# Kernel optimization log

Measured on AMD Instinct MI355X. Metric: run time of the kernel, lower is better.

The kernel has to match this reference:

```python
import jax, jax.numpy as jnp
import numpy as np

V = 100000
E = 1600000
BN_EPS = 1e-5


def spmm(edge_index, vals, X):
    # X: (V, Cin, B); sparse L @ X via scatter-add. y[r] += w * X[c]
    rows, cols = edge_index[0], edge_index[1]
    return jnp.zeros_like(X).at[rows].add(vals[:, None, None] * X[cols])


def cheb_conv(x, edge_index, vals, w, b=None):
    # x: (B, Cin, V), w: (K, Cin, Cout) -> (B, Cout, V)
    K = w.shape[0]
    x0 = jnp.transpose(x, (2, 1, 0))  # (V, Cin, B)
    xs = [x0]
    if K > 1:
        x1 = spmm(edge_index, vals, x0)
        xs.append(x1)
        for _ in range(2, K):
            x2 = 2.0 * spmm(edge_index, vals, x1) - x0
            xs.append(x2)
            x0, x1 = x1, x2
    xk = jnp.stack(xs)  # (K, V, Cin, B)
    out = jnp.einsum('kvcb,kco->bov', xk, w)
    if b is not None:
        out = out + b[None, :, None]
    return out


def batch_norm(x, g, b):
    # training-mode BatchNorm1d on (B, C, V): stats over (B, V), biased var
    m = jnp.mean(x, axis=(0, 2), keepdims=True)
    v = jnp.var(x, axis=(0, 2), keepdims=True)
    return g[None, :, None] * (x - m) * jax.lax.rsqrt(v + BN_EPS) + b[None, :, None]


def setup_inputs() -> dict:
    key = jax.random.key(0)
    ks = jax.random.split(key, 8)
    x = jax.random.normal(ks[0], (4, 32, V), dtype=jnp.float32)
    edge_index = jax.random.randint(ks[1], (2, E), 0, V, dtype=jnp.int32)
    # small values keep the K=4 Chebyshev recursion well-scaled
    lap_vals = 0.1 * jax.random.normal(ks[2], (E,), dtype=jnp.float32)
    def w(k, K, cin, cout):
        s = 1.0 / np.sqrt(K * cin)
        return s * jax.random.normal(k, (K, cin, cout), dtype=jnp.float32)
    return {
        'x': x, 'edge_index': edge_index, 'lap_vals': lap_vals,
        'in_bn_g': jnp.ones((32,), jnp.float32), 'in_bn_b': jnp.zeros((32,), jnp.float32),
        'in_w': w(ks[3], 4, 32, 64), 'in_b': jnp.zeros((64,), jnp.float32),
        'h0_bn_g': jnp.ones((64,), jnp.float32), 'h0_bn_b': jnp.zeros((64,), jnp.float32),
        'h0_w': w(ks[4], 4, 64, 64), 'h0_b': jnp.zeros((64,), jnp.float32),
        'h1_bn_g': jnp.ones((64,), jnp.float32), 'h1_bn_b': jnp.zeros((64,), jnp.float32),
        'h1_w': w(ks[5], 4, 64, 32), 'h1_b': jnp.zeros((32,), jnp.float32),
    }


def reference(x, edge_index, lap_vals, in_bn_g, in_bn_b, in_w, in_b,
              h0_bn_g, h0_bn_b, h0_w, h0_b, h1_bn_g, h1_bn_b, h1_w, h1_b):
    xn = batch_norm(x, in_bn_g, in_bn_b)
    out = cheb_conv(xn, edge_index, lap_vals, in_w, in_b)
    # hidden layer 0
    out = jax.nn.relu(out)
    out = batch_norm(out, h0_bn_g, h0_bn_b)
    out = cheb_conv(out, edge_index, lap_vals, h0_w, h0_b)
    # hidden layer 1
    out = jax.nn.relu(out)
    out = batch_norm(out, h1_bn_g, h1_bn_b)
    out = cheb_conv(out, edge_index, lap_vals, h1_w, h1_b)
    # in_channels == out_channels -> Identity shortcut on the BN'ed input
    return jax.nn.relu(out + xn)
```

## Files before the change

kernel.cpp:

```cpp
#include <hip/hip_runtime.h>
#include <cstdint>
#include <cstddef>

#define VN 100000
#define EN 1600000
static constexpr float BN_EPS_F = 1e-5f;
static constexpr float INV_N = 1.0f / 400000.0f;

using short8 = __attribute__((ext_vector_type(8))) short;
using f32x4  = __attribute__((ext_vector_type(4))) float;

__device__ __forceinline__ float bf_lo(unsigned int p) {
  return __builtin_bit_cast(float, p << 16);
}
__device__ __forceinline__ float bf_hi(unsigned int p) {
  return __builtin_bit_cast(float, p & 0xffff0000u);
}
__device__ __forceinline__ float bf1(unsigned short u) {
  return __builtin_bit_cast(float, ((unsigned int)u) << 16);
}
__device__ __forceinline__ unsigned short f2bf(float f) {
  unsigned int x = __builtin_bit_cast(unsigned int, f);
  x += 0x7fffu + ((x >> 16) & 1u);
  return (unsigned short)(x >> 16);
}
__device__ __forceinline__ unsigned int pack2(float a, float b) {
  return (unsigned int)f2bf(a) | ((unsigned int)f2bf(b) << 16);
}

template <int EPL, bool AX>
__device__ __forceinline__ void gather_accum(int start, int end,
    const int* __restrict__ cs, const float* __restrict__ vs,
    const unsigned short* __restrict__ X, int XS, int lane,
    float4 sc, float4 sh, float* acc) {
  int e = start;
  if constexpr (EPL == 4) {
    for (; e + 8 <= end; e += 8) {
      uint2 q[8]; float w[8];
#pragma unroll
      for (int u = 0; u < 8; u++) {
        q[u] = *reinterpret_cast<const uint2*>(X + (size_t)cs[e + u] * XS + lane * 4);
        w[u] = vs[e + u];
      }
#pragma unroll
      for (int u = 0; u < 8; u++) {
        float v0 = bf_lo(q[u].x), v1 = bf_hi(q[u].x), v2 = bf_lo(q[u].y), v3 = bf_hi(q[u].y);
        if constexpr (AX) {
          v0 = fmaxf(v0, 0.f) * sc.x + sh.x;
          v1 = fmaxf(v1, 0.f) * sc.y + sh.y;
          v2 = fmaxf(v2, 0.f) * sc.z + sh.z;
          v3 = fmaxf(v3, 0.f) * sc.w + sh.w;
        }
        acc[0] += w[u] * v0; acc[1] += w[u] * v1;
        acc[2] += w[u] * v2; acc[3] += w[u] * v3;
      }
    }
    for (; e + 4 <= end; e += 4) {
      uint2 q[4]; float w[4];
#pragma unroll
      for (int u = 0; u < 4; u++) {
        q[u] = *reinterpret_cast<const uint2*>(X + (size_t)cs[e + u] * XS + lane * 4);
        w[u] = vs[e + u];
      }
#pragma unroll
      for (int u = 0; u < 4; u++) {
        float v0 = bf_lo(q[u].x), v1 = bf_hi(q[u].x), v2 = bf_lo(q[u].y), v3 = bf_hi(q[u].y);
        if constexpr (AX) {
          v0 = fmaxf(v0, 0.f) * sc.x + sh.x;
          v1 = fmaxf(v1, 0.f) * sc.y + sh.y;
          v2 = fmaxf(v2, 0.f) * sc.z + sh.z;
          v3 = fmaxf(v3, 0.f) * sc.w + sh.w;
        }
        acc[0] += w[u] * v0; acc[1] += w[u] * v1;
        acc[2] += w[u] * v2; acc[3] += w[u] * v3;
      }
    }
    for (; e < end; e++) {
      const uint2 q = *reinterpret_cast<const uint2*>(X + (size_t)cs[e] * XS + lane * 4);
      const float w = vs[e];
      float v0 = bf_lo(q.x), v1 = bf_hi(q.x), v2 = bf_lo(q.y), v3 = bf_hi(q.y);
      if constexpr (AX) {
        v0 = fmaxf(v0, 0.f) * sc.x + sh.x;
        v1 = fmaxf(v1, 0.f) * sc.y + sh.y;
        v2 = fmaxf(v2, 0.f) * sc.z + sh.z;
        v3 = fmaxf(v3, 0.f) * sc.w + sh.w;
      }
      acc[0] += w * v0; acc[1] += w * v1; acc[2] += w * v2; acc[3] += w * v3;
    }
  } else {
    for (; e + 8 <= end; e += 8) {
      unsigned int q[8]; float w[8];
#pragma unroll
      for (int u = 0; u < 8; u++) {
        q[u] = *reinterpret_cast<const unsigned int*>(X + (size_t)cs[e + u] * XS + lane * 2);
        w[u] = vs[e + u];
      }
#pragma unroll
      for (int u = 0; u < 8; u++) {
        acc[0] += w[u] * bf_lo(q[u]);
        acc[1] += w[u] * bf_hi(q[u]);
      }
    }
    for (; e + 4 <= end; e += 4) {
      unsigned int q[4]; float w[4];
#pragma unroll
      for (int u = 0; u < 4; u++) {
        q[u] = *reinterpret_cast<const unsigned int*>(X + (size_t)cs[e + u] * XS + lane * 2);
        w[u] = vs[e + u];
      }
#pragma unroll
      for (int u = 0; u < 4; u++) {
        acc[0] += w[u] * bf_lo(q[u]);
        acc[1] += w[u] * bf_hi(q[u]);
      }
    }
    for (; e < end; e++) {
      const unsigned int q = *reinterpret_cast<const unsigned int*>(X + (size_t)cs[e] * XS + lane * 2);
      const float w = vs[e];
      acc[0] += w * bf_lo(q);
      acc[1] += w * bf_hi(q);
    }
  }
}

__global__ __launch_bounds__(256) void stats_x_kernel(const float* __restrict__ x,
                                                      float* __restrict__ stats) {
  const int p = blockIdx.x & 127;
  const int chunk = blockIdx.x >> 7;
  const int c = p & 31, b = p >> 5;
  const float* base = x + ((size_t)b * 32 + c) * VN + chunk * 12500;
  float s = 0.f, s2 = 0.f;
  for (int i = threadIdx.x; i < 12500; i += 256) {
    float v = base[i];
    s += v; s2 += v * v;
  }
  __shared__ float r1[256], r2[256];
  r1[threadIdx.x] = s; r2[threadIdx.x] = s2;
  __syncthreads();
  for (int off = 128; off > 0; off >>= 1) {
    if (threadIdx.x < off) {
      r1[threadIdx.x] += r1[threadIdx.x + off];
      r2[threadIdx.x] += r2[threadIdx.x + off];
    }
    __syncthreads();
  }
  if (threadIdx.x == 0) {
    atomicAdd(&stats[c], r1[0]);
    atomicAdd(&stats[64 + c], r2[0]);
  }
}

__global__ void finalize_stats_kernel(float* __restrict__ stats,
                                      const float* __restrict__ g,
                                      const float* __restrict__ beta, int C) {
  int c = threadIdx.x;
  if (c < C) {
    float m = stats[c] * INV_N;
    float var = stats[64 + c] * INV_N - m * m;
    float sc = g[c] * rsqrtf(var + BN_EPS_F);
    stats[128 + c] = sc;
    stats[192 + c] = beta[c] - m * sc;
  }
}

__global__ __launch_bounds__(128) void bn_transpose_kernel(const float* __restrict__ x,
                                                           const float* __restrict__ stats,
                                                           unsigned short* __restrict__ xn) {
  const int tid = threadIdx.x;
  const int b = tid >> 5, c = tid & 31;
  const int v0 = blockIdx.x * 64;
  const float sc = stats[128 + c], sh = stats[192 + c];
  const float* src = x + ((size_t)b * 32 + c) * VN;
  for (int i = 0; i < 64; i++) {
    int v = v0 + i;
    if (v < VN) xn[(size_t)v * 128 + tid] = f2bf(sc * src[v] + sh);
  }
}

__global__ __launch_bounds__(256) void pack_wb_kernel(const float* __restrict__ W,
                                                      unsigned short* __restrict__ Wb,
                                                      int Cin, int Cout) {
  const int i = blockIdx.x * 256 + threadIdx.x;
  const int KC = Cin >> 5, T = Cout >> 4;
  const int tot = 4 * KC * T * 512;
  if (i >= tot) return;
  const int j = i & 7;
  const int l = (i >> 3) & 63;
  const int rem = i >> 9;
  const int t = rem % T;
  const int kc = (rem / T) % KC;
  const int k = rem / (T * KC);
  const int c = kc * 32 + (l >> 4) * 8 + j;
  const int o = t * 16 + (l & 15);
  Wb[i] = f2bf(W[((size_t)k * Cin + c) * Cout + o]);
}

__global__ __launch_bounds__(256) void hist_kernel(const int* __restrict__ rows,
                                                   int* __restrict__ cnt) {
  int i = blockIdx.x * blockDim.x + threadIdx.x;
  const int stride = gridDim.x * blockDim.x;
  for (; i < EN; i += stride) atomicAdd(&cnt[rows[i]], 1);
}

__global__ __launch_bounds__(256) void scan1_kernel(const int* __restrict__ cnt,
                                                    int* __restrict__ rp,
                                                    int* __restrict__ chunkSums) {
  __shared__ int sh[256];
  const int t = threadIdx.x;
  const int base = blockIdx.x * 2048 + t * 8;
  int vals[8]; int tot = 0;
#pragma unroll
  for (int i = 0; i < 8; i++) {
    int idx = base + i;
    int v = (idx < VN) ? cnt[idx] : 0;
    vals[i] = v; tot += v;
  }
  sh[t] = tot;
  __syncthreads();
  for (int off = 1; off < 256; off <<= 1) {
    int v = (t >= off) ? sh[t - off] : 0;
    __syncthreads();
    sh[t] += v;
    __syncthreads();
  }
  int run = sh[t] - tot;
#pragma unroll
  for (int i = 0; i < 8; i++) {
    int idx = base + i;
    if (idx < VN) rp[idx] = run;
    run += vals[i];
  }
  if (t == 255) chunkSums[blockIdx.x] = sh[255];
}

__global__ void scan2_kernel(const int* __restrict__ chunkSums,
                             int* __restrict__ chunkOff,
                             int* __restrict__ rp, int nChunks) {
  if (threadIdx.x == 0 && blockIdx.x == 0) {
    int off = 0;
    for (int j = 0; j < nChunks; j++) { chunkOff[j] = off; off += chunkSums[j]; }
    rp[VN] = off;
  }
}

__global__ __launch_bounds__(256) void scan3_kernel(int* __restrict__ rp,
                                                    const int* __restrict__ chunkOff,
                                                    int* __restrict__ fill) {
  int i = blockIdx.x * 256 + threadIdx.x;
  if (i < VN) {
    int v = rp[i] + chunkOff[i >> 11];
    rp[i] = v;
    fill[i] = v;
  }
}

__global__ __launch_bounds__(256) void fill_kernel(const int* __restrict__ rows,
                                                   const int* __restrict__ cols,
                                                   const float* __restrict__ lap,
                                                   int* __restrict__ fill,
                                                   int* __restrict__ cols_s,
                                                   float* __restrict__ vals_s) {
  int i = blockIdx.x * blockDim.x + threadIdx.x;
  const int stride = gridDim.x * blockDim.x;
  for (; i < EN; i += stride) {
    int r = rows[i];
    int pos = atomicAdd(&fill[r], 1);
    cols_s[pos] = cols[i];
    vals_s[pos] = lap[i];
  }
}

template <int EPL, int MODE, bool AX, bool AP>
__global__ __launch_bounds__(256, 8) void spmm_kernel(const int* __restrict__ rp,
                                                   const int* __restrict__ cs,
                                                   const float* __restrict__ vs,
                                                   const unsigned short* __restrict__ X, int XS,
                                                   const unsigned short* __restrict__ P, int PS,
                                                   const unsigned short* __restrict__ Q, int QS,
                                                   unsigned short* __restrict__ Y, int YS,
                                                   const float* __restrict__ bnp) {
  const int lane = threadIdx.x & 63;
  const int row = blockIdx.x * 4 + (threadIdx.x >> 6);
  const int start = rp[row], end = rp[row + 1];
  float4 sc = {0.f, 0.f, 0.f, 0.f}, sh = {0.f, 0.f, 0.f, 0.f};
  if constexpr (AX || AP) {
    const int c0 = (lane * 4) & 63;
    sc = *reinterpret_cast<const float4*>(bnp + c0);
    sh = *reinterpret_cast<const float4*>(bnp + 64 + c0);
  }
  float acc[EPL];
#pragma unroll
  for (int j = 0; j < EPL; j++) acc[j] = 0.f;
  gather_accum<EPL, AX>(start, end, cs, vs, X, XS, lane, sc, sh, acc);

  if constexpr (EPL == 4) {
    float r0 = acc[0], r1 = acc[1], r2 = acc[2], r3 = acc[3];
    if constexpr (MODE == 1) {
      const uint2 p = *reinterpret_cast<const uint2*>(P + (size_t)row * PS + lane * 4);
      float p0 = bf_lo(p.x), p1 = bf_hi(p.x), p2 = bf_lo(p.y), p3 = bf_hi(p.y);
      if constexpr (AP) {
        p0 = fmaxf(p0, 0.f) * sc.x + sh.x;
        p1 = fmaxf(p1, 0.f) * sc.y + sh.y;
        p2 = fmaxf(p2, 0.f) * sc.z + sh.z;
        p3 = fmaxf(p3, 0.f) * sc.w + sh.w;
      }
      r0 = 2.f * r0 - p0;
      r1 = 2.f * r1 - p1;
      r2 = 2.f * r2 - p2;
      r3 = 2.f * r3 - p3;
    }
    uint2 r;
    r.x = pack2(r0, r1);
    r.y = pack2(r2, r3);
    *reinterpret_cast<uint2*>(Y + (size_t)row * YS + lane * 4) = r;
  } else {
    float r0 = acc[0], r1 = acc[1];
    if constexpr (MODE == 1) {
      const unsigned int p = *reinterpret_cast<const unsigned int*>(P + (size_t)row * PS + lane * 2);
      r0 = 2.f * r0 - bf_lo(p);
      r1 = 2.f * r1 - bf_hi(p);
    } else if constexpr (MODE == 2) {
      const unsigned int p = *reinterpret_cast<const unsigned int*>(P + (size_t)row * PS + lane * 2);
      r0 = 2.f * r0 + bf_lo(p);
      r1 = 2.f * r1 + bf_hi(p);
    } else if constexpr (MODE == 3) {
      const unsigned int p = *reinterpret_cast<const unsigned int*>(P + (size_t)row * PS + lane * 2);
      const unsigned int qq = *reinterpret_cast<const unsigned int*>(Q + (size_t)row * QS + lane * 2);
      r0 = 2.f * r0 - bf_lo(qq) + bf_lo(p);
      r1 = 2.f * r1 - bf_hi(qq) + bf_hi(p);
    } else if constexpr (MODE == 4) {
      const unsigned int p = *reinterpret_cast<const unsigned int*>(P + (size_t)row * PS + lane * 2);
      const unsigned int qq = *reinterpret_cast<const unsigned int*>(Q + (size_t)row * QS + lane * 2);
      r0 = r0 - bf_lo(qq) + bf_lo(p);
      r1 = r1 - bf_hi(qq) + bf_hi(p);
    }
    *reinterpret_cast<unsigned int*>(Y + (size_t)row * YS + lane * 2) = pack2(r0, r1);
  }
}

template <int Cin, int Cout, int X0S, int X1S, int X2S, bool AFF0>
__global__ __launch_bounds__(256, 8) void fused_cheb_kernel(const int* __restrict__ rp,
                                                         const int* __restrict__ cs,
                                                         const float* __restrict__ vs,
                                                         const unsigned short* __restrict__ X0,
                                                         const unsigned short* __restrict__ X1,
                                                         const unsigned short* __restrict__ X2,
                                                         unsigned short* __restrict__ OUT,
                                                         const unsigned short* __restrict__ Wb,
                                                         const float* __restrict__ Bias,
                                                         const float* __restrict__ bnp) {
  constexpr int EPL = Cin * 4 / 64;
  constexpr int ROWSH = Cin * 4;
  __shared__ unsigned short t3s[4 * ROWSH];
  const int lane = threadIdx.x & 63;
  const int wv = threadIdx.x >> 6;
  const int row0 = blockIdx.x * 4;
  const int row = row0 + wv;

  float g[EPL];
#pragma unroll
  for (int j = 0; j < EPL; j++) g[j] = 0.f;
  const int start = rp[row], end = rp[row + 1];
  const float4 z4 = {0.f, 0.f, 0.f, 0.f};
  gather_accum<EPL, false>(start, end, cs, vs, X2, X2S, lane, z4, z4, g);
  {
    unsigned int* tw = reinterpret_cast<unsigned int*>(t3s + wv * ROWSH);
    if constexpr (EPL == 4) {
      const uint2 p = *reinterpret_cast<const uint2*>(X1 + (size_t)row * X1S + lane * 4);
      tw[lane * 2]     = pack2(2.f * g[0] - bf_lo(p.x), 2.f * g[1] - bf_hi(p.x));
      tw[lane * 2 + 1] = pack2(2.f * g[2] - bf_lo(p.y), 2.f * g[3] - bf_hi(p.y));
    } else {
      const unsigned int p = *reinterpret_cast<const unsigned int*>(X1 + (size_t)row * X1S + lane * 2);
      tw[lane] = pack2(2.f * g[0] - bf_lo(p), 2.f * g[1] - bf_hi(p));
    }
  }
  __syncthreads();

  constexpr int KC = Cin / 32;
  constexpr int T = Cout / 16;
  const int col = lane & 15, quad = lane >> 4;
  const int t = wv % T;
  const int ar = col >> 2, ab = col & 3;

  const unsigned short* xa0 = X0 + (size_t)(row0 + ar) * X0S + ab * Cin + quad * 8;
  const unsigned short* xa1 = X1 + (size_t)(row0 + ar) * X1S + ab * Cin + quad * 8;
  const unsigned short* xa2 = X2 + (size_t)(row0 + ar) * X2S + ab * Cin + quad * 8;
  const unsigned short* wb = Wb + (size_t)t * 512 + lane * 8;

  f32x4 acc = {0.f, 0.f, 0.f, 0.f};
#pragma unroll
  for (int kc = 0; kc < KC; kc++) {
    short8 af;
    if constexpr (AFF0) {
      const short8 raw = *reinterpret_cast<const short8*>(xa0 + kc * 32);
      const int cb = quad * 8 + kc * 32;
      const float4 s0 = *reinterpret_cast<const float4*>(bnp + cb);
      const float4 s1 = *reinterpret_cast<const float4*>(bnp + cb + 4);
      const float4 t0 = *reinterpret_cast<const float4*>(bnp + 64 + cb);
      const float4 t1 = *reinterpret_cast<const float4*>(bnp + 64 + cb + 4);
      const float scv[8] = {s0.x, s0.y, s0.z, s0.w, s1.x, s1.y, s1.z, s1.w};
      const float shv[8] = {t0.x, t0.y, t0.z, t0.w, t1.x, t1.y, t1.z, t1.w};
#pragma unroll
      for (int j = 0; j < 8; j++) {
        float v = fmaxf(bf1((unsigned short)raw[j]), 0.f) * scv[j] + shv[j];
        af[j] = (short)f2bf(v);
      }
    } else {
      af = *reinterpret_cast<const short8*>(xa0 + kc * 32);
    }
    const short8 bf = *reinterpret_cast<const short8*>(wb + (size_t)(0 * KC + kc) * T * 512);
    acc = __builtin_amdgcn_mfma_f32_16x16x32_bf16(af, bf, acc, 0, 0, 0);
  }
#pragma unroll
  for (int kc = 0; kc < KC; kc++) {
    const short8 af = *reinterpret_cast<const short8*>(xa1 + kc * 32);
    const short8 bf = *reinterpret_cast<const short8*>(wb + (size_t)(1 * KC + kc) * T * 512);
    acc = __builtin_amdgcn_mfma_f32_16x16x32_bf16(af, bf, acc, 0, 0, 0);
  }
#pragma unroll
  for (int kc = 0; kc < KC; kc++) {
    const short8 af = *reinterpret_cast<const short8*>(xa2 + kc * 32);
    const short8 bf = *reinterpret_cast<const short8*>(wb + (size_t)(2 * KC + kc) * T * 512);
    acc = __builtin_amdgcn_mfma_f32_16x16x32_bf16(af, bf, acc, 0, 0, 0);
  }
#pragma unroll
  for (int kc = 0; kc < KC; kc++) {
    const short8 af = *reinterpret_cast<const short8*>(&t3s[ar * ROWSH + ab * Cin + kc * 32 + quad * 8]);
    const short8 bf = *reinterpret_cast<const short8*>(wb + (size_t)(3 * KC + kc) * T * 512);
    acc = __builtin_amdgcn_mfma_f32_16x16x32_bf16(af, bf, acc, 0, 0, 0);
  }
  __syncthreads();

  if (T == 4 || wv < 2) {
    const int og = t * 16 + col;
    const float bs = Bias[og];
#pragma unroll
    for (int r = 0; r < 4; r++) {
      OUT[(size_t)(row0 + quad) * 256 + r * Cout + og] = f2bf(acc[r] + bs);
    }
  }
}

__global__ __launch_bounds__(256, 8) void gemm_z_kernel(const unsigned short* __restrict__ A,
                                                        const unsigned short* __restrict__ Wb,
                                                        const float* __restrict__ Bias,
                                                        unsigned short* __restrict__ zA,
                                                        unsigned short* __restrict__ zB,
                                                        const float* __restrict__ bnp) {
  const int lane = threadIdx.x & 63;
  const int wv = threadIdx.x >> 6;
  const int row0 = blockIdx.x * 4;
  const int col = lane & 15, quad = lane >> 4;
  const int ar = col >> 2, ab = col & 3;
  const unsigned short* xa = A + (size_t)(row0 + ar) * 256 + ab * 64 + quad * 8;
  const unsigned short* wb = Wb + (size_t)wv * 4 * 512 + lane * 8;
  unsigned short* zr = (wv < 2) ? (zA + (size_t)wv * VN * 128)
                                : (zB + (size_t)(wv - 2) * VN * 128);
  short8 afr[2];
#pragma unroll
  for (int kc = 0; kc < 2; kc++) {
    const short8 raw = *reinterpret_cast<const short8*>(xa + kc * 32);
    const int cb = quad * 8 + kc * 32;
    const float4 s0 = *reinterpret_cast<const float4*>(bnp + cb);
    const float4 s1 = *reinterpret_cast<const float4*>(bnp + cb + 4);
    const float4 t0 = *reinterpret_cast<const float4*>(bnp + 64 + cb);
    const float4 t1 = *reinterpret_cast<const float4*>(bnp + 64 + cb + 4);
    const float scv[8] = {s0.x, s0.y, s0.z, s0.w, s1.x, s1.y, s1.z, s1.w};
    const float shv[8] = {t0.x, t0.y, t0.z, t0.w, t1.x, t1.y, t1.z, t1.w};
#pragma unroll
    for (int j = 0; j < 8; j++) {
      float v = fmaxf(bf1((unsigned short)raw[j]), 0.f) * scv[j] + shv[j];
      afr[kc][j] = (short)f2bf(v);
    }
  }
#pragma unroll
  for (int t = 0; t < 2; t++) {
    f32x4 acc = {0.f, 0.f, 0.f, 0.f};
#pragma unroll
    for (int kc = 0; kc < 2; kc++) {
      const short8 bf = *reinterpret_cast<const short8*>(wb + (size_t)(kc * 2 + t) * 512);
      acc = __builtin_amdgcn_mfma_f32_16x16x32_bf16(afr[kc], bf, acc, 0, 0, 0);
    }
    const int og = t * 16 + col;
    const float bs = (wv == 0) ? Bias[og] : 0.f;
#pragma unroll
    for (int r = 0; r < 4; r++) {
      zr[(size_t)(row0 + quad) * 128 + r * 32 + og] = f2bf(acc[r] + bs);
    }
  }
}

__global__ __launch_bounds__(256) void stats_out_kernel(const unsigned short* __restrict__ SRC,
                                                        float* __restrict__ stats) {
  const int tid = threadIdx.x;
  const int per = (VN + gridDim.x - 1) / gridDim.x;
  const int v0 = blockIdx.x * per;
  const int v1 = (v0 + per < VN) ? (v0 + per) : VN;
  float s = 0.f, s2 = 0.f;
  for (int v = v0; v < v1; v++) {
    float val = bf1(SRC[(size_t)v * 256 + tid]);
    val = fmaxf(val, 0.f);
    s += val; s2 += val * val;
  }
  __shared__ float r1[256], r2[256];
  r1[tid] = s; r2[tid] = s2;
  __syncthreads();
  if (tid < 64) {
    float a = r1[tid] + r1[tid + 64] + r1[tid + 128] + r1[tid + 192];
    float b = r2[tid] + r2[tid + 64] + r2[tid + 128] + r2[tid + 192];
    atomicAdd(&stats[tid], a);
    atomicAdd(&stats[64 + tid], b);
  }
}

__global__ __launch_bounds__(256) void final_kernel(const unsigned short* __restrict__ SRC,
                                                    const unsigned short* __restrict__ xn,
                                                    float* __restrict__ out) {
  const int lane = threadIdx.x & 63;
  const int grp = threadIdx.x >> 6;
  const int v = blockIdx.x * 64 + lane;
  if (v >= VN) return;
  for (int ob = grp; ob < 128; ob += 4) {
    float val = bf1(SRC[(size_t)v * 128 + ob]) + bf1(xn[(size_t)v * 128 + ob]);
    val = fmaxf(val, 0.f);
    out[(size_t)ob * VN + v] = val;
  }
}

static constexpr size_t align_up(size_t x) { return (x + 255) & ~(size_t)255; }
static constexpr size_t OFF_RP    = 0;
static constexpr size_t OFF_FILL  = align_up(OFF_RP + (size_t)(VN + 1) * 4);
static constexpr size_t OFF_CHS   = align_up(OFF_FILL + (size_t)VN * 4);
static constexpr size_t OFF_CHO   = align_up(OFF_CHS + 256);
static constexpr size_t OFF_STATS = align_up(OFF_CHO + 256);
static constexpr size_t OFF_WP    = align_up(OFF_STATS + 1024);
static constexpr size_t OFF_CS    = align_up(OFF_WP + 32768 * 2);
static constexpr size_t OFF_VS    = align_up(OFF_CS + (size_t)EN * 4);
static constexpr size_t OFF_XN    = align_up(OFF_VS + (size_t)EN * 4);
static constexpr size_t OFF_XL    = align_up(OFF_XN + (size_t)VN * 128 * 2);
static constexpr size_t OFF_A     = align_up(OFF_XL + (size_t)VN * 256 * 2);
static constexpr size_t OFF_B     = align_up(OFF_A + (size_t)VN * 256 * 2);
static constexpr size_t OFF_END   = OFF_B + (size_t)VN * 256 * 2;

extern "C" void kernel_launch(void* const* d_in, const int* in_sizes, int n_in,
                              void* d_out, int out_size, void* d_ws, size_t ws_size,
                              hipStream_t stream) {
  if (ws_size < OFF_END) return;

  const float* x       = (const float*)d_in[0];
  const int*   rows    = (const int*)d_in[1];
  const int*   cols    = rows + EN;
  const float* lap     = (const float*)d_in[2];
  const float* in_bn_g = (const float*)d_in[3];
  const float* in_bn_b = (const float*)d_in[4];
  const float* in_w    = (const float*)d_in[5];
  const float* in_b    = (const float*)d_in[6];
  const float* h0_bn_g = (const float*)d_in[7];
  const float* h0_bn_b = (const float*)d_in[8];
  const float* h0_w    = (const float*)d_in[9];
  const float* h0_b    = (const float*)d_in[10];
  const float* h1_bn_g = (const float*)d_in[11];
  const float* h1_bn_b = (const float*)d_in[12];
  const float* h1_w    = (const float*)d_in[13];
  const float* h1_b    = (const float*)d_in[14];
  float* outp = (float*)d_out;

  char* ws = (char*)d_ws;
  int*   rp     = (int*)(ws + OFF_RP);
  int*   fill   = (int*)(ws + OFF_FILL);
  int*   chS    = (int*)(ws + OFF_CHS);
  int*   chO    = (int*)(ws + OFF_CHO);
  float* stats  = (float*)(ws + OFF_STATS);
  unsigned short* wbIn = (unsigned short*)(ws + OFF_WP);
  unsigned short* wbH0 = wbIn + 8192;
  unsigned short* wbH1 = wbH0 + 16384;
  int*   cs     = (int*)(ws + OFF_CS);
  float* vs     = (float*)(ws + OFF_VS);
  unsigned short* xn = (unsigned short*)(ws + OFF_XN);
  unsigned short* XL = (unsigned short*)(ws + OFF_XL);
  unsigned short* A  = (unsigned short*)(ws + OFF_A);
  unsigned short* B  = (unsigned short*)(ws + OFF_B);
  const float* bnp = stats + 128;

  const int nChunks = (VN + 2047) / 2048;

  pack_wb_kernel<<<32, 256, 0, stream>>>(in_w, wbIn, 32, 64);
  pack_wb_kernel<<<64, 256, 0, stream>>>(h0_w, wbH0, 64, 64);
  pack_wb_kernel<<<32, 256, 0, stream>>>(h1_w, wbH1, 64, 32);

  hipMemsetAsync(stats, 0, 1024, stream);
  stats_x_kernel<<<1024, 256, 0, stream>>>(x, stats);
  finalize_stats_kernel<<<1, 64, 0, stream>>>(stats, in_bn_g, in_bn_b, 32);
  bn_transpose_kernel<<<1563, 128, 0, stream>>>(x, stats, xn);

  hipMemsetAsync(fill, 0, (size_t)VN * 4, stream);
  hist_kernel<<<2048, 256, 0, stream>>>(rows, fill);
  scan1_kernel<<<nChunks, 256, 0, stream>>>(fill, rp, chS);
  scan2_kernel<<<1, 64, 0, stream>>>(chS, chO, rp, nChunks);
  scan3_kernel<<<(VN + 255) / 256, 256, 0, stream>>>(rp, chO, fill);
  fill_kernel<<<2048, 256, 0, stream>>>(rows, cols, lap, fill, cs, vs);

  unsigned short* XLa = XL;
  unsigned short* XLb = XL + (size_t)VN * 128;
  spmm_kernel<2, 0, false, false><<<VN / 4, 256, 0, stream>>>(
      rp, cs, vs, xn, 128, nullptr, 0, nullptr, 0, XLa, 128, nullptr);
  spmm_kernel<2, 1, false, false><<<VN / 4, 256, 0, stream>>>(
      rp, cs, vs, XLa, 128, xn, 128, nullptr, 0, XLb, 128, nullptr);
  fused_cheb_kernel<32, 64, 128, 128, 128, false><<<VN / 4, 256, 0, stream>>>(
      rp, cs, vs, xn, XLa, XLb, A, wbIn, in_b, nullptr);
  hipMemsetAsync(stats, 0, 1024, stream);
  stats_out_kernel<<<256, 256, 0, stream>>>(A, stats);
  finalize_stats_kernel<<<1, 64, 0, stream>>>(stats, h0_bn_g, h0_bn_b, 64);

  spmm_kernel<4, 0, true, false><<<VN / 4, 256, 0, stream>>>(
      rp, cs, vs, A, 256, nullptr, 0, nullptr, 0, XL, 256, bnp);
  spmm_kernel<4, 1, false, true><<<VN / 4, 256, 0, stream>>>(
      rp, cs, vs, XL, 256, A, 256, nullptr, 0, B, 256, bnp);
  fused_cheb_kernel<64, 64, 256, 256, 256, true><<<VN / 4, 256, 0, stream>>>(
      rp, cs, vs, A, XL, B, A, wbH0, h0_b, bnp);
  hipMemsetAsync(stats, 0, 1024, stream);
  stats_out_kernel<<<256, 256, 0, stream>>>(A, stats);
  finalize_stats_kernel<<<1, 64, 0, stream>>>(stats, h1_bn_g, h1_bn_b, 64);

  {
    unsigned short* z0 = XL;
    unsigned short* z1 = XL + (size_t)VN * 128;
    unsigned short* z2 = B;
    unsigned short* z3 = B + (size_t)VN * 128;
    gemm_z_kernel<<<VN / 4, 256, 0, stream>>>(A, wbH1, h1_b, z0, z2, bnp);
    spmm_kernel<2, 2, false, false><<<VN / 4, 256, 0, stream>>>(
        rp, cs, vs, z3, 128, z2, 128, nullptr, 0, z2, 128, nullptr);
    spmm_kernel<2, 3, false, false><<<VN / 4, 256, 0, stream>>>(
        rp, cs, vs, z2, 128, z1, 128, z3, 128, z1, 128, nullptr);
    spmm_kernel<2, 4, false, false><<<VN / 4, 256, 0, stream>>>(
        rp, cs, vs, z1, 128, z0, 128, z2, 128, z0, 128, nullptr);
    final_kernel<<<1563, 256, 0, stream>>>(z0, xn, outp);
  }
}
```

Baseline: 1.611 ms.

## Apply BN affine after SpMM via row sums and store post-ReLU activations

ReLU moves into the producer GEMM epilogue, so stored activations are already rectified. The per-channel BN scale and shift then factor out of the sparse gather as sc*sum(w*x) + rowsum*sh, with a new kernel precomputing Laplacian row sums. This removes per-edge fmax/fma work in the gather loop. The gather loop is also simplified from 8-way plus 4-way unrolling to 4-way only, which may reduce memory-level parallelism. The rowsum buffer aliases the fill workspace.

```diff
diff --git a/kernel.cpp b/kernel.cpp
--- a/kernel.cpp
+++ b/kernel.cpp
@@ -28,97 +28,45 @@
   return (unsigned int)f2bf(a) | ((unsigned int)f2bf(b) << 16);
 }
 
-template <int EPL, bool AX>
+template <int EPL>
 __device__ __forceinline__ void gather_accum(int start, int end,
     const int* __restrict__ cs, const float* __restrict__ vs,
-    const unsigned short* __restrict__ X, int XS, int lane,
-    float4 sc, float4 sh, float* acc) {
+    const unsigned short* __restrict__ X, int XS, int lane, float* acc) {
   int e = start;
-  if constexpr (EPL == 4) {
-    for (; e + 8 <= end; e += 8) {
-      uint2 q[8]; float w[8];
-#pragma unroll
-      for (int u = 0; u < 8; u++) {
-        q[u] = *reinterpret_cast<const uint2*>(X + (size_t)cs[e + u] * XS + lane * 4);
-        w[u] = vs[e + u];
-      }
-#pragma unroll
-      for (int u = 0; u < 8; u++) {
-        float v0 = bf_lo(q[u].x), v1 = bf_hi(q[u].x), v2 = bf_lo(q[u].y), v3 = bf_hi(q[u].y);
-        if constexpr (AX) {
-          v0 = fmaxf(v0, 0.f) * sc.x + sh.x;
-          v1 = fmaxf(v1, 0.f) * sc.y + sh.y;
-          v2 = fmaxf(v2, 0.f) * sc.z + sh.z;
-          v3 = fmaxf(v3, 0.f) * sc.w + sh.w;
-        }
-        acc[0] += w[u] * v0; acc[1] += w[u] * v1;
-        acc[2] += w[u] * v2; acc[3] += w[u] * v3;
-      }
-    }
-    for (; e + 4 <= end; e += 4) {
-      uint2 q[4]; float w[4];
-#pragma unroll
-      for (int u = 0; u < 4; u++) {
-        q[u] = *reinterpret_cast<const uint2*>(X + (size_t)cs[e + u] * XS + lane * 4);
-        w[u] = vs[e + u];
-      }
-#pragma unroll
-      for (int u = 0; u < 4; u++) {
-        float v0 = bf_lo(q[u].x), v1 = bf_hi(q[u].x), v2 = bf_lo(q[u].y), v3 = bf_hi(q[u].y);
-        if constexpr (AX) {
-          v0 = fmaxf(v0, 0.f) * sc.x + sh.x;
-          v1 = fmaxf(v1, 0.f) * sc.y + sh.y;
-          v2 = fmaxf(v2, 0.f) * sc.z + sh.z;
-          v3 = fmaxf(v3, 0.f) * sc.w + sh.w;
-        }
-        acc[0] += w[u] * v0; acc[1] += w[u] * v1;
-        acc[2] += w[u] * v2; acc[3] += w[u] * v3;
-      }
-    }
-    for (; e < end; e++) {
-      const uint2 q = *reinterpret_cast<const uint2*>(X + (size_t)cs[e] * XS + lane * 4);
-      const float w = vs[e];
-      float v0 = bf_lo(q.x), v1 = bf_hi(q.x), v2 = bf_lo(q.y), v3 = bf_hi(q.y);
-      if constexpr (AX) {
-        v0 = fmaxf(v0, 0.f) * sc.x + sh.x;
-        v1 = fmaxf(v1, 0.f) * sc.y + sh.y;
-        v2 = fmaxf(v2, 0.f) * sc.z + sh.z;
-        v3 = fmaxf(v3, 0.f) * sc.w + sh.w;
-      }
-      acc[0] += w * v0; acc[1] += w * v1; acc[2] += w * v2; acc[3] += w * v3;
-    }
-  } else {
-    for (; e + 8 <= end; e += 8) {
-      unsigned int q[8]; float w[8];
-#pragma unroll
-      for (int u = 0; u < 8; u++) {
-        q[u] = *reinterpret_cast<const unsigned int*>(X + (size_t)cs[e + u] * XS + lane * 2);
-        w[u] = vs[e + u];
-      }
-#pragma unroll
-      for (int u = 0; u < 8; u++) {
-        acc[0] += w[u] * bf_lo(q[u]);
-        acc[1] += w[u] * bf_hi(q[u]);
-      }
-    }
-    for (; e + 4 <= end; e += 4) {
-      unsigned int q[4]; float w[4];
-#pragma unroll
-      for (int u = 0; u < 4; u++) {
-        q[u] = *reinterpret_cast<const unsigned int*>(X + (size_t)cs[e + u] * XS + lane * 2);
-        w[u] = vs[e + u];
-      }
-#pragma unroll
-      for (int u = 0; u < 4; u++) {
-        acc[0] += w[u] * bf_lo(q[u]);
-        acc[1] += w[u] * bf_hi(q[u]);
-      }
-    }
-    for (; e < end; e++) {
-      const unsigned int q = *reinterpret_cast<const unsigned int*>(X + (size_t)cs[e] * XS + lane * 2);
-      const float w = vs[e];
-      acc[0] += w * bf_lo(q);
-      acc[1] += w * bf_hi(q);
+  for (; e + 4 <= end; e += 4) {
+    const int c0 = cs[e], c1 = cs[e + 1], c2 = cs[e + 2], c3 = cs[e + 3];
+    const float w0 = vs[e], w1 = vs[e + 1], w2 = vs[e + 2], w3 = vs[e + 3];
+    if constexpr (EPL == 4) {
+      const uint2 q0 = *reinterpret_cast<const uint2*>(X + (size_t)c0 * XS + lane * 4);
+      const uint2 q1 = *reinterpret_cast<const uint2*>(X + (size_t)c1 * XS + lane * 4);
+      const uint2 q2 = *reinterpret_cast<const uint2*>(X + (size_t)c2 * XS + lane * 4);
+      const uint2 q3 = *reinterpret_cast<const uint2*>(X + (size_t)c3 * XS + lane * 4);
+      acc[0] += w0 * bf_lo(q0.x) + w1 * bf_lo(q1.x) + w2 * bf_lo(q2.x) + w3 * bf_lo(q3.x);
+      acc[1] += w0 * bf_hi(q0.x) + w1 * bf_hi(q1.x) + w2 * bf_hi(q2.x) + w3 * bf_hi(q3.x);
+      acc[2] += w0 * bf_lo(q0.y) + w1 * bf_lo(q1.y) + w2 * bf_lo(q2.y) + w3 * bf_lo(q3.y);
+      acc[3] += w0 * bf_hi(q0.y) + w1 * bf_hi(q1.y) + w2 * bf_hi(q2.y) + w3 * bf_hi(q3.y);
+    } else {
+      const unsigned int q0 = *reinterpret_cast<const unsigned int*>(X + (size_t)c0 * XS + lane * 2);
+      const unsigned int q1 = *reinterpret_cast<const unsigned int*>(X + (size_t)c1 * XS + lane * 2);
+      const unsigned int q2 = *reinterpret_cast<const unsigned int*>(X + (size_t)c2 * XS + lane * 2);
+      const unsigned int q3 = *reinterpret_cast<const unsigned int*>(X + (size_t)c3 * XS + lane * 2);
+      acc[0] += w0 * bf_lo(q0) + w1 * bf_lo(q1) + w2 * bf_lo(q2) + w3 * bf_lo(q3);
+      acc[1] += w0 * bf_hi(q0) + w1 * bf_hi(q1) + w2 * bf_hi(q2) + w3 * bf_hi(q3);
+    }
+  }
+  for (; e < end; e++) {
+    const int c0 = cs[e];
+    const float w0 = vs[e];
+    if constexpr (EPL == 4) {
+      const uint2 q0 = *reinterpret_cast<const uint2*>(X + (size_t)c0 * XS + lane * 4);
+      acc[0] += w0 * bf_lo(q0.x);
+      acc[1] += w0 * bf_hi(q0.x);
+      acc[2] += w0 * bf_lo(q0.y);
+      acc[3] += w0 * bf_hi(q0.y);
+    } else {
+      const unsigned int q0 = *reinterpret_cast<const unsigned int*>(X + (size_t)c0 * XS + lane * 2);
+      acc[0] += w0 * bf_lo(q0);
+      acc[1] += w0 * bf_hi(q0);
     }
   }
 }
@@ -270,7 +218,18 @@
   }
 }
 
-template <int EPL, int MODE, bool AX, bool AP>
+__global__ __launch_bounds__(256) void row_sum_kernel(const int* __restrict__ rp,
+                                                      const float* __restrict__ vs,
+                                                      float* __restrict__ rowsum) {
+  const int i = blockIdx.x * 256 + threadIdx.x;
+  if (i >= VN) return;
+  const int s = rp[i], e = rp[i + 1];
+  float acc = 0.f;
+  for (int j = s; j < e; j++) acc += vs[j];
+  rowsum[i] = acc;
+}
+
+template <int EPL, int MODE, bool AFFE, bool AFFP>
 __global__ __launch_bounds__(256, 8) void spmm_kernel(const int* __restrict__ rp,
                                                    const int* __restrict__ cs,
                                                    const float* __restrict__ vs,
@@ -278,31 +237,39 @@
                                                    const unsigned short* __restrict__ P, int PS,
                                                    const unsigned short* __restrict__ Q, int QS,
                                                    unsigned short* __restrict__ Y, int YS,
-                                                   const float* __restrict__ bnp) {
+                                                   const float* __restrict__ bnp,
+                                                   const float* __restrict__ rowsum) {
   const int lane = threadIdx.x & 63;
   const int row = blockIdx.x * 4 + (threadIdx.x >> 6);
   const int start = rp[row], end = rp[row + 1];
-  float4 sc = {0.f, 0.f, 0.f, 0.f}, sh = {0.f, 0.f, 0.f, 0.f};
-  if constexpr (AX || AP) {
-    const int c0 = (lane * 4) & 63;
-    sc = *reinterpret_cast<const float4*>(bnp + c0);
-    sh = *reinterpret_cast<const float4*>(bnp + 64 + c0);
-  }
   float acc[EPL];
 #pragma unroll
   for (int j = 0; j < EPL; j++) acc[j] = 0.f;
-  gather_accum<EPL, AX>(start, end, cs, vs, X, XS, lane, sc, sh, acc);
+  gather_accum<EPL>(start, end, cs, vs, X, XS, lane, acc);
 
   if constexpr (EPL == 4) {
+    float4 sc, sh;
+    if constexpr (AFFE || AFFP) {
+      const int c0 = (lane * 4) & 63;
+      sc = *reinterpret_cast<const float4*>(bnp + c0);
+      sh = *reinterpret_cast<const float4*>(bnp + 64 + c0);
+    }
     float r0 = acc[0], r1 = acc[1], r2 = acc[2], r3 = acc[3];
+    if constexpr (AFFE) {
+      const float rs = rowsum[row];
+      r0 = sc.x * r0 + rs * sh.x;
+      r1 = sc.y * r1 + rs * sh.y;
+      r2 = sc.z * r2 + rs * sh.z;
+      r3 = sc.w * r3 + rs * sh.w;
+    }
     if constexpr (MODE == 1) {
       const uint2 p = *reinterpret_cast<const uint2*>(P + (size_t)row * PS + lane * 4);
       float p0 = bf_lo(p.x), p1 = bf_hi(p.x), p2 = bf_lo(p.y), p3 = bf_hi(p.y);
-      if constexpr (AP) {
-        p0 = fmaxf(p0, 0.f) * sc.x + sh.x;
-        p1 = fmaxf(p1, 0.f) * sc.y + sh.y;
-        p2 = fmaxf(p2, 0.f) * sc.z + sh.z;
-        p3 = fmaxf(p3, 0.f) * sc.w + sh.w;
+      if constexpr (AFFP) {
+        p0 = p0 * sc.x + sh.x;
+        p1 = p1 * sc.y + sh.y;
+        p2 = p2 * sc.z + sh.z;
+        p3 = p3 * sc.w + sh.w;
       }
       r0 = 2.f * r0 - p0;
       r1 = 2.f * r1 - p1;
@@ -361,8 +328,7 @@
 #pragma unroll
   for (int j = 0; j < EPL; j++) g[j] = 0.f;
   const int start = rp[row], end = rp[row + 1];
-  const float4 z4 = {0.f, 0.f, 0.f, 0.f};
-  gather_accum<EPL, false>(start, end, cs, vs, X2, X2S, lane, z4, z4, g);
+  gather_accum<EPL>(start, end, cs, vs, X2, X2S, lane, g);
   {
     unsigned int* tw = reinterpret_cast<unsigned int*>(t3s + wv * ROWSH);
     if constexpr (EPL == 4) {
@@ -402,7 +368,7 @@
       const float shv[8] = {t0.x, t0.y, t0.z, t0.w, t1.x, t1.y, t1.z, t1.w};
 #pragma unroll
       for (int j = 0; j < 8; j++) {
-        float v = fmaxf(bf1((unsigned short)raw[j]), 0.f) * scv[j] + shv[j];
+        float v = bf1((unsigned short)raw[j]) * scv[j] + shv[j];
         af[j] = (short)f2bf(v);
       }
     } else {
@@ -436,7 +402,8 @@
     const float bs = Bias[og];
 #pragma unroll
     for (int r = 0; r < 4; r++) {
-      OUT[(size_t)(row0 + quad) * 256 + r * Cout + og] = f2bf(acc[r] + bs);
+      const float val = fmaxf(acc[r] + bs, 0.f);
+      OUT[(size_t)(row0 + quad) * 256 + r * Cout + og] = f2bf(val);
     }
   }
 }
@@ -469,7 +436,7 @@
     const float shv[8] = {t0.x, t0.y, t0.z, t0.w, t1.x, t1.y, t1.z, t1.w};
 #pragma unroll
     for (int j = 0; j < 8; j++) {
-      float v = fmaxf(bf1((unsigned short)raw[j]), 0.f) * scv[j] + shv[j];
+      float v = bf1((unsigned short)raw[j]) * scv[j] + shv[j];
       afr[kc][j] = (short)f2bf(v);
     }
   }
@@ -499,7 +466,6 @@
   float s = 0.f, s2 = 0.f;
   for (int v = v0; v < v1; v++) {
     float val = bf1(SRC[(size_t)v * 256 + tid]);
-    val = fmaxf(val, 0.f);
     s += val; s2 += val * val;
   }
   __shared__ float r1[256], r2[256];
@@ -568,6 +534,7 @@
   char* ws = (char*)d_ws;
   int*   rp     = (int*)(ws + OFF_RP);
   int*   fill   = (int*)(ws + OFF_FILL);
+  float* rowsum = (float*)(ws + OFF_FILL);
   int*   chS    = (int*)(ws + OFF_CHS);
   int*   chO    = (int*)(ws + OFF_CHO);
   float* stats  = (float*)(ws + OFF_STATS);
@@ -599,13 +566,14 @@
   scan2_kernel<<<1, 64, 0, stream>>>(chS, chO, rp, nChunks);
   scan3_kernel<<<(VN + 255) / 256, 256, 0, stream>>>(rp, chO, fill);
   fill_kernel<<<2048, 256, 0, stream>>>(rows, cols, lap, fill, cs, vs);
+  row_sum_kernel<<<(VN + 255) / 256, 256, 0, stream>>>(rp, vs, rowsum);
 
   unsigned short* XLa = XL;
   unsigned short* XLb = XL + (size_t)VN * 128;
   spmm_kernel<2, 0, false, false><<<VN / 4, 256, 0, stream>>>(
-      rp, cs, vs, xn, 128, nullptr, 0, nullptr, 0, XLa, 128, nullptr);
+      rp, cs, vs, xn, 128, nullptr, 0, nullptr, 0, XLa, 128, nullptr, nullptr);
   spmm_kernel<2, 1, false, false><<<VN / 4, 256, 0, stream>>>(
-      rp, cs, vs, XLa, 128, xn, 128, nullptr, 0, XLb, 128, nullptr);
+      rp, cs, vs, XLa, 128, xn, 128, nullptr, 0, XLb, 128, nullptr, nullptr);
   fused_cheb_kernel<32, 64, 128, 128, 128, false><<<VN / 4, 256, 0, stream>>>(
       rp, cs, vs, xn, XLa, XLb, A, wbIn, in_b, nullptr);
   hipMemsetAsync(stats, 0, 1024, stream);
@@ -613,9 +581,9 @@
   finalize_stats_kernel<<<1, 64, 0, stream>>>(stats, h0_bn_g, h0_bn_b, 64);
 
   spmm_kernel<4, 0, true, false><<<VN / 4, 256, 0, stream>>>(
-      rp, cs, vs, A, 256, nullptr, 0, nullptr, 0, XL, 256, bnp);
+      rp, cs, vs, A, 256, nullptr, 0, nullptr, 0, XL, 256, bnp, rowsum);
   spmm_kernel<4, 1, false, true><<<VN / 4, 256, 0, stream>>>(
-      rp, cs, vs, XL, 256, A, 256, nullptr, 0, B, 256, bnp);
+      rp, cs, vs, XL, 256, A, 256, nullptr, 0, B, 256, bnp, nullptr);
   fused_cheb_kernel<64, 64, 256, 256, 256, true><<<VN / 4, 256, 0, stream>>>(
       rp, cs, vs, A, XL, B, A, wbH0, h0_b, bnp);
   hipMemsetAsync(stats, 0, 1024, stream);
@@ -629,11 +597,11 @@
     unsigned short* z3 = B + (size_t)VN * 128;
     gemm_z_kernel<<<VN / 4, 256, 0, stream>>>(A, wbH1, h1_b, z0, z2, bnp);
     spmm_kernel<2, 2, false, false><<<VN / 4, 256, 0, stream>>>(
-        rp, cs, vs, z3, 128, z2, 128, nullptr, 0, z2, 128, nullptr);
+        rp, cs, vs, z3, 128, z2, 128, nullptr, 0, z2, 128, nullptr, nullptr);
     spmm_kernel<2, 3, false, false><<<VN / 4, 256, 0, stream>>>(
-        rp, cs, vs, z2, 128, z1, 128, z3, 128, z1, 128, nullptr);
+        rp, cs, vs, z2, 128, z1, 128, z3, 128, z1, 128, nullptr, nullptr);
     spmm_kernel<2, 4, false, false><<<VN / 4, 256, 0, stream>>>(
-        rp, cs, vs, z1, 128, z0, 128, z2, 128, z0, 128, nullptr);
+        rp, cs, vs, z1, 128, z0, 128, z2, 128, z0, 128, nullptr, nullptr);
     final_kernel<<<1563, 256, 0, stream>>>(z0, xn, outp);
   }
 }
```

After: 1.665 ms. +3.3%, slower.
